# Kernel tuning notes

Hardware: AMD Instinct MI355X
Metric: run time of the kernel (lower is better)

The kernel has to match this reference:

```python
import jax, jax.numpy as jnp
import numpy as np

B, S, E, H = 2, 1024, 1024, 16
Dh = E // H


def setup_inputs() -> dict:
    key = jax.random.key(0)
    ks = jax.random.split(key, 32)
    sc = 1.0 / np.sqrt(E)  # xavier-ish scale
    inp = {}
    names_x = ["x_q_a", "x_q_b", "x_kv_a", "x_kv_b"]
    for i, n in enumerate(names_x):
        inp[n] = jax.random.normal(ks[i], (B, S, E), jnp.float32)
    # causal mask, broadcastable to (B, H, S, S); masked where == 0
    inp["mask"] = jnp.tril(jnp.ones((S, S), jnp.int32))[None, None, :, :]
    inp["layer_theta"] = jnp.float32(0.3)
    inp["thetas_head"] = 0.1 * jax.random.normal(ks[4], (H,), jnp.float32)
    i = 5
    for p in ["q", "k", "v", "o"]:
        inp[p + "_wa"] = sc * jax.random.normal(ks[i], (E, E), jnp.float32); i += 1
        inp[p + "_wb"] = sc * jax.random.normal(ks[i], (E, E), jnp.float32); i += 1
        inp[p + "_ba"] = jnp.zeros((E,), jnp.float32)
        inp[p + "_bb"] = jnp.zeros((E,), jnp.float32)
    return inp


def _qc_dense(xa, xb, wa, wb, ba, bb, j2):
    # F.linear: x @ W.T + b ; j2 is a scalar so (Wb*j2) factors out
    out_a = xa @ wa.T + ba + (xb @ wb.T) * j2
    out_b = xa @ wb.T + bb + xb @ wa.T
    return out_a, out_b


def _shape(x):
    # (B,S,E) -> (B,H,S,Dh)
    return x.reshape(B, S, H, Dh).transpose(0, 2, 1, 3)


def _unshape(x):
    return x.transpose(0, 2, 1, 3).reshape(B, S, E)


def _rope(x):
    # standard rotate-half RoPE on last dim, positions over axis -2
    inv_freq = 1.0 / (10000.0 ** (jnp.arange(0, Dh, 2, dtype=jnp.float32) / Dh))
    ang = jnp.arange(S, dtype=jnp.float32)[:, None] * inv_freq[None, :]  # (S, Dh/2)
    cos = jnp.concatenate([jnp.cos(ang), jnp.cos(ang)], axis=-1)  # (S, Dh)
    sin = jnp.concatenate([jnp.sin(ang), jnp.sin(ang)], axis=-1)
    x1, x2 = x[..., : Dh // 2], x[..., Dh // 2:]
    rot = jnp.concatenate([-x2, x1], axis=-1)
    return x * cos + rot * sin


def reference(x_q_a, x_q_b, x_kv_a, x_kv_b, mask, layer_theta, thetas_head,
              q_wa, q_wb, q_ba, q_bb, k_wa, k_wb, k_ba, k_bb,
              v_wa, v_wb, v_ba, v_bb, o_wa, o_wb, o_ba, o_bb):
    j2 = jnp.sin(2.0 * layer_theta) - 1.0
    qa, qb = _qc_dense(x_q_a, x_q_b, q_wa, q_wb, q_ba, q_bb, j2)
    ka, kb = _qc_dense(x_kv_a, x_kv_b, k_wa, k_wb, k_ba, k_bb, j2)
    va, vb = _qc_dense(x_kv_a, x_kv_b, v_wa, v_wb, v_ba, v_bb, j2)
    qa, qb = _rope(_shape(qa)), _rope(_shape(qb))
    ka, kb = _rope(_shape(ka)), _rope(_shape(kb))
    va, vb = _shape(va), _shape(vb)
    j2h = (jnp.sin(2.0 * thetas_head) - 1.0).reshape(1, H, 1, 1)
    # dual QC score matrices (B,H,S,S)
    s_a = jnp.einsum("bhqd,bhkd->bhqk", qa, ka) + jnp.einsum("bhqd,bhkd->bhqk", qb, kb) * j2h
    s_b = jnp.einsum("bhqd,bhkd->bhqk", qa, kb) + jnp.einsum("bhqd,bhkd->bhqk", qb, ka)
    mag = jnp.sqrt(s_a * s_a + s_b * s_b + 1e-8) / np.sqrt(Dh)
    mag = jnp.where(mask == 0, -1e9, mag)
    attn = jax.nn.softmax(mag, axis=-1)
    out_a = _unshape(jnp.einsum("bhqk,bhkd->bhqd", attn, va))
    out_b = _unshape(jnp.einsum("bhqk,bhkd->bhqd", attn, vb))
    return _qc_dense(out_a, out_b, o_wa, o_wb, o_ba, o_bb, j2)
```

## Files before the change

kernel.cpp:

```cpp
#include <hip/hip_runtime.h>
#include <math.h>
#include <stdint.h>

#define BATCH 2
#define SEQ   1024
#define EMB   1024
#define NH    16
#define DH    64
#define BSE   (BATCH*SEQ*EMB)
#define MROWS (BATCH*SEQ)

typedef unsigned short u16;
typedef __attribute__((ext_vector_type(8))) short short8;
typedef __attribute__((ext_vector_type(4))) float f32x4;

__device__ __forceinline__ float bf2f(u16 u) {
    return __uint_as_float(((unsigned int)u) << 16);
}
__device__ __forceinline__ u16 f2bf(float f) {
    unsigned int x = __float_as_uint(f);
    x += 0x7FFFu + ((x >> 16) & 1u);
    return (u16)(x >> 16);
}

__device__ __forceinline__ void async_copy16(const void* g, void* l) {
    __builtin_amdgcn_global_load_lds(
        (const __attribute__((address_space(1))) unsigned int*)g,
        (__attribute__((address_space(3))) unsigned int*)l,
        16, 0, 0);
}

struct PackArgs {
    const float* src[16];
    u16*         dst[16];
    int          n[16];
    int          scaled[16];
};

__global__ __launch_bounds__(256) void pack_kernel(PackArgs pa, const float* __restrict__ theta)
{
    const int e = blockIdx.y;
    const int i = (blockIdx.x * 256 + threadIdx.x) * 4;
    if (i >= pa.n[e]) return;
    float sc = 1.0f;
    if (pa.scaled[e]) sc = sinf(2.0f * theta[0]) - 1.0f;
    float4 v = *(const float4*)(pa.src[e] + i);
    u16* d = pa.dst[e] + i;
    ushort4 o;
    o.x = f2bf(v.x * sc); o.y = f2bf(v.y * sc);
    o.z = f2bf(v.z * sc); o.w = f2bf(v.w * sc);
    *(ushort4*)d = o;
}

struct GemmArgs {
    const u16*   A1;
    const u16*   A2;
    const u16*   Blo[4];
    const u16*   Bhi[4];
    const float* bias[4];
    void*        dst[4];
    int          mode[4];
};

__global__ __launch_bounds__(256) void mfma_gemm(GemmArgs ga)
{
    __shared__ u16 sA[128][32];
    __shared__ u16 sB[128][32];

    const int t    = threadIdx.x;
    const int lane = t & 63;
    const int w    = t >> 6;
    const int wx   = w & 1;
    const int wy   = w >> 1;
    const int n0   = blockIdx.x * 128;
    const int m0   = blockIdx.y * 128;
    const int seg  = n0 >> 10;
    const int nloc = n0 & 1023;

    const int srow = t >> 2;
    const int sb   = (t & 3) * 16;

    f32x4 acc[4][4] = {};

    const char* A1 = (const char*)ga.A1;
    const char* A2 = (const char*)ga.A2;
    const char* Bl = (const char*)ga.Blo[seg];
    const char* Bh = (const char*)ga.Bhi[seg];

    const int frow = lane & 15;
    const int quad = lane >> 4;

    for (int kt = 0; kt < 64; ++kt) {
        const char* As = (kt & 32) ? A2 : A1;
        const char* Bs = (kt & 32) ? Bh : Bl;
        const size_t kbyte = (size_t)(kt & 31) * 64;

        __syncthreads();
        #pragma unroll
        for (int r = 0; r < 2; ++r) {
            const int row = r*64 + srow;
            const int ldsoff = (r*64 + w*16) * 64;
            async_copy16(As + (size_t)(m0 + row)*2048 + kbyte + sb,
                         (char*)&sA[0][0] + ldsoff);
            async_copy16(Bs + (size_t)(nloc + row)*2048 + kbyte + sb,
                         (char*)&sB[0][0] + ldsoff);
        }
        __syncthreads();

        short8 af[4], bfr[4];
        #pragma unroll
        for (int i = 0; i < 4; ++i)
            af[i] = *(const short8*)&sA[wy*64 + i*16 + frow][quad*8];
        #pragma unroll
        for (int j = 0; j < 4; ++j)
            bfr[j] = *(const short8*)&sB[wx*64 + j*16 + frow][quad*8];

        #pragma unroll
        for (int i = 0; i < 4; ++i)
            #pragma unroll
            for (int j = 0; j < 4; ++j)
                acc[i][j] = __builtin_amdgcn_mfma_f32_16x16x32_bf16(
                                af[i], bfr[j], acc[i][j], 0, 0, 0);
    }

    const float* bias = ga.bias[seg];
    const int mode = ga.mode[seg];
    #pragma unroll
    for (int j = 0; j < 4; ++j) {
        const int c = nloc + wx*64 + j*16 + frow;
        const float bv = bias[c];
        #pragma unroll
        for (int i = 0; i < 4; ++i) {
            #pragma unroll
            for (int reg = 0; reg < 4; ++reg) {
                const int m = m0 + wy*64 + i*16 + quad*4 + reg;
                const float val = acc[i][j][reg] + bv;
                if (mode == 1) {
                    ((float*)ga.dst[seg])[(size_t)m*1024 + c] = val;
                } else if (mode == 2) {
                    ((u16*)ga.dst[seg])[((size_t)(m >> 10) << 20) + (size_t)c*1024 + (m & 1023)] = f2bf(val);
                } else {
                    ((u16*)ga.dst[seg])[(size_t)m*1024 + c] = f2bf(val);
                }
            }
        }
    }
}

__global__ __launch_bounds__(256) void rope_kernel(
    u16* qa, u16* qb, u16* ka, u16* kb)
{
    u16* p;
    switch (blockIdx.y) {
        case 0:  p = qa; break;
        case 1:  p = qb; break;
        case 2:  p = ka; break;
        default: p = kb; break;
    }
    const int i   = blockIdx.x * 256 + threadIdx.x;
    const int d   = i & 31;
    const int hh  = (i >> 5) & (NH - 1);
    const int row = i >> 9;
    const int s   = row & (SEQ - 1);
    const size_t base = (size_t)row * EMB + hh * DH;

    float x1 = bf2f(p[base + d]);
    float x2 = bf2f(p[base + d + 32]);
    const float invf = expf(-(float)d * (9.210340371976184f / 32.0f));
    const float ang  = (float)s * invf;
    float sn, cs;
    sincosf(ang, &sn, &cs);
    p[base + d]      = f2bf(x1 * cs - x2 * sn);
    p[base + d + 32] = f2bf(x2 * cs + x1 * sn);
}

__global__ __launch_bounds__(256) void attn_mfma(
    const u16* __restrict__ qa, const u16* __restrict__ qb,
    const u16* __restrict__ ka, const u16* __restrict__ kb,
    const u16* __restrict__ vat, const u16* __restrict__ vbt,
    const float* __restrict__ thetas,
    u16* __restrict__ oa, u16* __restrict__ ob)
{
    __shared__ u16 sKa[64][64];
    __shared__ u16 sKb[64][64];
    __shared__ u16 sVa[64][64];
    __shared__ u16 sVb[64][64];
    __shared__ u16 sP[4][16][72];

    const int t    = threadIdx.x;
    const int lane = t & 63;
    const int w    = t >> 6;
    const int L15  = lane & 15;
    const int quad = lane >> 4;

    const int bid  = blockIdx.x;
    const int aa   = (bid >> 5) & 7;
    const int qt   = (bid >> 8) ? aa : (15 - aa);
    const int bh   = bid & 31;
    const int h    = bh & 15;
    const int b    = bh >> 4;

    const float j2h = sinf(2.0f * thetas[h]) - 1.0f;

    const int   qrow  = qt*64 + w*16 + L15;
    const size_t qbase = (size_t)(b*SEQ + qrow) * EMB + h*DH;
    short8 fqa[2], fqb[2], fjqb[2];
    fqa[0] = *(const short8*)(qa + qbase + quad*8);
    fqa[1] = *(const short8*)(qa + qbase + 32 + quad*8);
    fqb[0] = *(const short8*)(qb + qbase + quad*8);
    fqb[1] = *(const short8*)(qb + qbase + 32 + quad*8);
    #pragma unroll
    for (int s2 = 0; s2 < 2; ++s2) {
        short8 src = fqb[s2], dst;
        #pragma unroll
        for (int j = 0; j < 8; ++j)
            dst[j] = (short)f2bf(bf2f((u16)src[j]) * j2h);
        fjqb[s2] = dst;
    }

    f32x4 acc_a[4] = {};
    f32x4 acc_b[4] = {};
    float m_run[4] = {-1e30f, -1e30f, -1e30f, -1e30f};
    float l_run[4] = {0.f, 0.f, 0.f, 0.f};

    const int subrow = lane >> 3;
    const int g      = (lane & 7) ^ subrow;
    const int swz    = L15 & 7;

    for (int kt = 0; kt <= qt; ++kt) {
        __syncthreads();
        #pragma unroll
        for (int i = 0; i < 2; ++i) {
            const int row = w*16 + i*8 + subrow;
            const int ldsoff = (w*16 + i*8) * 128;
            const size_t ktok = (size_t)(b*SEQ + kt*64 + row);
            async_copy16((const char*)ka + ktok*2048 + h*128 + g*16,
                         (char*)&sKa[0][0] + ldsoff);
            async_copy16((const char*)kb + ktok*2048 + h*128 + g*16,
                         (char*)&sKb[0][0] + ldsoff);
            const size_t vrow = (size_t)b*1048576 + (size_t)(h*64 + row)*1024 + kt*64;
            async_copy16((const char*)vat + vrow*2 + g*16,
                         (char*)&sVa[0][0] + ldsoff);
            async_copy16((const char*)vbt + vrow*2 + g*16,
                         (char*)&sVb[0][0] + ldsoff);
        }
        __syncthreads();

        f32x4 sa[4] = {}, sb[4] = {};
        #pragma unroll
        for (int n = 0; n < 4; ++n) {
            const u16* rKa = &sKa[n*16 + L15][0];
            const u16* rKb = &sKb[n*16 + L15][0];
            short8 ka0 = *(const short8*)(rKa + (( quad      ^ swz) << 3));
            short8 ka1 = *(const short8*)(rKa + (((4 + quad) ^ swz) << 3));
            short8 kb0 = *(const short8*)(rKb + (( quad      ^ swz) << 3));
            short8 kb1 = *(const short8*)(rKb + (((4 + quad) ^ swz) << 3));
            sa[n] = __builtin_amdgcn_mfma_f32_16x16x32_bf16(fqa[0],  ka0, sa[n], 0, 0, 0);
            sa[n] = __builtin_amdgcn_mfma_f32_16x16x32_bf16(fqa[1],  ka1, sa[n], 0, 0, 0);
            sa[n] = __builtin_amdgcn_mfma_f32_16x16x32_bf16(fjqb[0], kb0, sa[n], 0, 0, 0);
            sa[n] = __builtin_amdgcn_mfma_f32_16x16x32_bf16(fjqb[1], kb1, sa[n], 0, 0, 0);
            sb[n] = __builtin_amdgcn_mfma_f32_16x16x32_bf16(fqa[0],  kb0, sb[n], 0, 0, 0);
            sb[n] = __builtin_amdgcn_mfma_f32_16x16x32_bf16(fqa[1],  kb1, sb[n], 0, 0, 0);
            sb[n] = __builtin_amdgcn_mfma_f32_16x16x32_bf16(fqb[0],  ka0, sb[n], 0, 0, 0);
            sb[n] = __builtin_amdgcn_mfma_f32_16x16x32_bf16(fqb[1],  ka1, sb[n], 0, 0, 0);
        }

        float mag[4][4];
        #pragma unroll
        for (int n = 0; n < 4; ++n)
            #pragma unroll
            for (int r = 0; r < 4; ++r) {
                const float A = sa[n][r], B = sb[n][r];
                mag[n][r] = sqrtf(A*A + B*B + 1e-8f) * 0.125f;
            }
        if (kt == qt) {
            #pragma unroll
            for (int n = 0; n < 4; ++n)
                #pragma unroll
                for (int r = 0; r < 4; ++r)
                    if (n*16 + L15 > w*16 + quad*4 + r) mag[n][r] = -1e9f;
        }

        float rmax[4], psum[4], alpha[4];
        #pragma unroll
        for (int r = 0; r < 4; ++r) {
            float mx = fmaxf(fmaxf(mag[0][r], mag[1][r]), fmaxf(mag[2][r], mag[3][r]));
            #pragma unroll
            for (int off = 8; off >= 1; off >>= 1)
                mx = fmaxf(mx, __shfl_xor(mx, off, 64));
            rmax[r] = mx;
        }
        float p[4][4];
        #pragma unroll
        for (int r = 0; r < 4; ++r) {
            const float m_new = fmaxf(m_run[r], rmax[r]);
            alpha[r] = expf(m_run[r] - m_new);
            m_run[r] = m_new;
            float ps = 0.f;
            #pragma unroll
            for (int n = 0; n < 4; ++n) {
                p[n][r] = expf(mag[n][r] - m_new);
                ps += p[n][r];
            }
            #pragma unroll
            for (int off = 8; off >= 1; off >>= 1)
                ps += __shfl_xor(ps, off, 64);
            psum[r] = ps;
            l_run[r] = l_run[r] * alpha[r] + psum[r];
        }
        #pragma unroll
        for (int n = 0; n < 4; ++n)
            #pragma unroll
            for (int r = 0; r < 4; ++r) {
                acc_a[n][r] *= alpha[r];
                acc_b[n][r] *= alpha[r];
            }

        #pragma unroll
        for (int n = 0; n < 4; ++n)
            #pragma unroll
            for (int r = 0; r < 4; ++r)
                sP[w][quad*4 + r][n*16 + L15] = f2bf(p[n][r]);

        short8 pf0 = *(const short8*)&sP[w][L15][quad*8];
        short8 pf1 = *(const short8*)&sP[w][L15][32 + quad*8];

        #pragma unroll
        for (int n = 0; n < 4; ++n) {
            const u16* rVa = &sVa[n*16 + L15][0];
            const u16* rVb = &sVb[n*16 + L15][0];
            short8 va0 = *(const short8*)(rVa + (( quad      ^ swz) << 3));
            short8 va1 = *(const short8*)(rVa + (((4 + quad) ^ swz) << 3));
            short8 vb0 = *(const short8*)(rVb + (( quad      ^ swz) << 3));
            short8 vb1 = *(const short8*)(rVb + (((4 + quad) ^ swz) << 3));
            acc_a[n] = __builtin_amdgcn_mfma_f32_16x16x32_bf16(pf0, va0, acc_a[n], 0, 0, 0);
            acc_a[n] = __builtin_amdgcn_mfma_f32_16x16x32_bf16(pf1, va1, acc_a[n], 0, 0, 0);
            acc_b[n] = __builtin_amdgcn_mfma_f32_16x16x32_bf16(pf0, vb0, acc_b[n], 0, 0, 0);
            acc_b[n] = __builtin_amdgcn_mfma_f32_16x16x32_bf16(pf1, vb1, acc_b[n], 0, 0, 0);
        }
    }

    float inv[4];
    #pragma unroll
    for (int r = 0; r < 4; ++r) inv[r] = 1.0f / l_run[r];
    #pragma unroll
    for (int reg = 0; reg < 4; ++reg) {
        const size_t tok = (size_t)(b*SEQ + qt*64 + w*16 + quad*4 + reg);
        #pragma unroll
        for (int n = 0; n < 4; ++n) {
            const size_t idx = tok*EMB + h*DH + n*16 + L15;
            oa[idx] = f2bf(acc_a[n][reg] * inv[reg]);
            ob[idx] = f2bf(acc_b[n][reg] * inv[reg]);
        }
    }
}

extern "C" void kernel_launch(void* const* d_in, const int* in_sizes, int n_in,
                              void* d_out, int out_size, void* d_ws, size_t ws_size,
                              hipStream_t stream)
{
    const float* x_q_a  = (const float*)d_in[0];
    const float* x_q_b  = (const float*)d_in[1];
    const float* x_kv_a = (const float*)d_in[2];
    const float* x_kv_b = (const float*)d_in[3];
    const float* theta    = (const float*)d_in[5];
    const float* thetas_h = (const float*)d_in[6];
    const float* q_wa = (const float*)d_in[7];
    const float* q_wb = (const float*)d_in[8];
    const float* q_ba = (const float*)d_in[9];
    const float* q_bb = (const float*)d_in[10];
    const float* k_wa = (const float*)d_in[11];
    const float* k_wb = (const float*)d_in[12];
    const float* k_ba = (const float*)d_in[13];
    const float* k_bb = (const float*)d_in[14];
    const float* v_wa = (const float*)d_in[15];
    const float* v_wb = (const float*)d_in[16];
    const float* v_ba = (const float*)d_in[17];
    const float* v_bb = (const float*)d_in[18];
    const float* o_wa = (const float*)d_in[19];
    const float* o_wb = (const float*)d_in[20];
    const float* o_ba = (const float*)d_in[21];
    const float* o_bb = (const float*)d_in[22];

    u16* W = (u16*)d_ws;
    const size_t XN = (size_t)BSE;
    const size_t WN = (size_t)EMB*EMB;
    u16* xq_a16  = W;
    u16* xq_b16  = W + XN;
    u16* xkv_a16 = W + 2*XN;
    u16* xkv_b16 = W + 3*XN;
    u16* wbase   = W + 4*XN;
    u16* q_wa16  = wbase;
    u16* q_wb16  = wbase + WN;
    u16* k_wa16  = wbase + 2*WN;
    u16* k_wb16  = wbase + 3*WN;
    u16* v_wa16  = wbase + 4*WN;
    u16* v_wb16  = wbase + 5*WN;
    u16* o_wa16  = wbase + 6*WN;
    u16* o_wb16  = wbase + 7*WN;
    u16* q_wbs16 = wbase + 8*WN;
    u16* k_wbs16 = wbase + 9*WN;
    u16* v_wbs16 = wbase + 10*WN;
    u16* o_wbs16 = wbase + 11*WN;
    u16* qkv     = wbase + 12*WN;
    u16* qa16 = qkv;
    u16* qb16 = qkv + XN;
    u16* ka16 = qkv + 2*XN;
    u16* kb16 = qkv + 3*XN;
    u16* vat16 = qkv + 4*XN;
    u16* vbt16 = qkv + 5*XN;
    u16* ao16 = xq_a16;
    u16* bo16 = xq_b16;

    float* out_a = (float*)d_out;
    float* out_b = out_a + (size_t)BSE;

    PackArgs pa;
    const float* psrc[16] = { x_q_a, x_q_b, x_kv_a, x_kv_b,
                              q_wa, q_wb, k_wa, k_wb, v_wa, v_wb, o_wa, o_wb,
                              q_wb, k_wb, v_wb, o_wb };
    u16* pdst[16] = { xq_a16, xq_b16, xkv_a16, xkv_b16,
                      q_wa16, q_wb16, k_wa16, k_wb16, v_wa16, v_wb16, o_wa16, o_wb16,
                      q_wbs16, k_wbs16, v_wbs16, o_wbs16 };
    for (int e = 0; e < 16; ++e) {
        pa.src[e] = psrc[e];
        pa.dst[e] = pdst[e];
        pa.n[e]   = (e < 4) ? (int)XN : (int)WN;
        pa.scaled[e] = (e >= 12) ? 1 : 0;
    }
    pack_kernel<<<dim3(XN/(256*4), 16), 256, 0, stream>>>(pa, theta);

    GemmArgs g1;
    g1.A1 = xq_a16; g1.A2 = xq_b16;
    g1.Blo[0] = q_wa16;  g1.Bhi[0] = q_wbs16; g1.bias[0] = q_ba; g1.dst[0] = qa16; g1.mode[0] = 0;
    g1.Blo[1] = q_wb16;  g1.Bhi[1] = q_wa16;  g1.bias[1] = q_bb; g1.dst[1] = qb16; g1.mode[1] = 0;
    g1.Blo[2] = q_wa16;  g1.Bhi[2] = q_wa16;  g1.bias[2] = q_ba; g1.dst[2] = qa16; g1.mode[2] = 0;
    g1.Blo[3] = q_wa16;  g1.Bhi[3] = q_wa16;  g1.bias[3] = q_ba; g1.dst[3] = qa16; g1.mode[3] = 0;
    mfma_gemm<<<dim3(16, MROWS/128), 256, 0, stream>>>(g1);

    GemmArgs g2;
    g2.A1 = xkv_a16; g2.A2 = xkv_b16;
    g2.Blo[0] = k_wa16; g2.Bhi[0] = k_wbs16; g2.bias[0] = k_ba; g2.dst[0] = ka16;  g2.mode[0] = 0;
    g2.Blo[1] = k_wb16; g2.Bhi[1] = k_wa16;  g2.bias[1] = k_bb; g2.dst[1] = kb16;  g2.mode[1] = 0;
    g2.Blo[2] = v_wa16; g2.Bhi[2] = v_wbs16; g2.bias[2] = v_ba; g2.dst[2] = vat16; g2.mode[2] = 2;
    g2.Blo[3] = v_wb16; g2.Bhi[3] = v_wa16;  g2.bias[3] = v_bb; g2.dst[3] = vbt16; g2.mode[3] = 2;
    mfma_gemm<<<dim3(32, MROWS/128), 256, 0, stream>>>(g2);

    rope_kernel<<<dim3((BATCH*SEQ*NH*32)/256, 4), 256, 0, stream>>>(qa16, qb16, ka16, kb16);

    attn_mfma<<<BATCH*NH*(SEQ/64), 256, 0, stream>>>(qa16, qb16, ka16, kb16,
                                                     vat16, vbt16, thetas_h, ao16, bo16);

    GemmArgs g3;
    g3.A1 = ao16; g3.A2 = bo16;
    g3.Blo[0] = o_wa16; g3.Bhi[0] = o_wbs16; g3.bias[0] = o_ba; g3.dst[0] = out_a; g3.mode[0] = 1;
    g3.Blo[1] = o_wb16; g3.Bhi[1] = o_wa16;  g3.bias[1] = o_bb; g3.dst[1] = out_b; g3.mode[1] = 1;
    g3.Blo[2] = o_wa16; g3.Bhi[2] = o_wa16;  g3.bias[2] = o_ba; g3.dst[2] = out_a; g3.mode[2] = 1;
    g3.Blo[3] = o_wa16; g3.Bhi[3] = o_wa16;  g3.bias[3] = o_ba; g3.dst[3] = out_a; g3.mode[3] = 1;
    mfma_gemm<<<dim3(16, MROWS/128), 256, 0, stream>>>(g3);
}
```

Before: 355.4 us.

## Fuse RoPE into projection GEMM epilogue and merge Q/KV projection launches

Applies rotary embedding directly on the fp32 accumulators in the GEMM epilogue for the Q and K outputs, removing the separate rope kernel and its extra read/write pass over four bf16 tensors. GemmArgs now carries per-segment A operands, so the Q and KV projections run as one launch with 48 column segments. This cuts launch overhead and tail effects, at the cost of sincos work in the epilogue and a larger argument struct.

```diff
diff --git a/kernel.cpp b/kernel.cpp
--- a/kernel.cpp
+++ b/kernel.cpp
@@ -53,13 +53,13 @@
 }
 
 struct GemmArgs {
-    const u16*   A1;
-    const u16*   A2;
-    const u16*   Blo[4];
-    const u16*   Bhi[4];
-    const float* bias[4];
-    void*        dst[4];
-    int          mode[4];
+    const u16*   A1s[8];
+    const u16*   A2s[8];
+    const u16*   Blo[8];
+    const u16*   Bhi[8];
+    const float* bias[8];
+    void*        dst[8];
+    int          mode[8];
 };
 
 __global__ __launch_bounds__(256) void mfma_gemm(GemmArgs ga)
@@ -82,8 +82,8 @@
 
     f32x4 acc[4][4] = {};
 
-    const char* A1 = (const char*)ga.A1;
-    const char* A2 = (const char*)ga.A2;
+    const char* A1 = (const char*)ga.A1s[seg];
+    const char* A2 = (const char*)ga.A2s[seg];
     const char* Bl = (const char*)ga.Blo[seg];
     const char* Bh = (const char*)ga.Bhi[seg];
 
@@ -125,16 +125,48 @@
 
     const float* bias = ga.bias[seg];
     const int mode = ga.mode[seg];
+
     #pragma unroll
     for (int j = 0; j < 4; ++j) {
         const int c = nloc + wx*64 + j*16 + frow;
         const float bv = bias[c];
         #pragma unroll
+        for (int i = 0; i < 4; ++i)
+            #pragma unroll
+            for (int reg = 0; reg < 4; ++reg)
+                acc[i][j][reg] += bv;
+    }
+
+    if (mode == 3) {
+        #pragma unroll
+        for (int jj = 0; jj < 2; ++jj) {
+            const float invf = expf(-(float)(jj*16 + frow) * 0.28782313662425576f);
+            #pragma unroll
+            for (int i = 0; i < 4; ++i) {
+                #pragma unroll
+                for (int reg = 0; reg < 4; ++reg) {
+                    const int m = m0 + wy*64 + i*16 + quad*4 + reg;
+                    const float ang = (float)(m & (SEQ-1)) * invf;
+                    float sn, cs;
+                    sincosf(ang, &sn, &cs);
+                    const float x1 = acc[i][jj][reg];
+                    const float x2 = acc[i][jj+2][reg];
+                    acc[i][jj][reg]   = x1*cs - x2*sn;
+                    acc[i][jj+2][reg] = x2*cs + x1*sn;
+                }
+            }
+        }
+    }
+
+    #pragma unroll
+    for (int j = 0; j < 4; ++j) {
+        const int c = nloc + wx*64 + j*16 + frow;
+        #pragma unroll
         for (int i = 0; i < 4; ++i) {
             #pragma unroll
             for (int reg = 0; reg < 4; ++reg) {
                 const int m = m0 + wy*64 + i*16 + quad*4 + reg;
-                const float val = acc[i][j][reg] + bv;
+                const float val = acc[i][j][reg];
                 if (mode == 1) {
                     ((float*)ga.dst[seg])[(size_t)m*1024 + c] = val;
                 } else if (mode == 2) {
@@ -145,33 +177,6 @@
             }
         }
     }
-}
-
-__global__ __launch_bounds__(256) void rope_kernel(
-    u16* qa, u16* qb, u16* ka, u16* kb)
-{
-    u16* p;
-    switch (blockIdx.y) {
-        case 0:  p = qa; break;
-        case 1:  p = qb; break;
-        case 2:  p = ka; break;
-        default: p = kb; break;
-    }
-    const int i   = blockIdx.x * 256 + threadIdx.x;
-    const int d   = i & 31;
-    const int hh  = (i >> 5) & (NH - 1);
-    const int row = i >> 9;
-    const int s   = row & (SEQ - 1);
-    const size_t base = (size_t)row * EMB + hh * DH;
-
-    float x1 = bf2f(p[base + d]);
-    float x2 = bf2f(p[base + d + 32]);
-    const float invf = expf(-(float)d * (9.210340371976184f / 32.0f));
-    const float ang  = (float)s * invf;
-    float sn, cs;
-    sincosf(ang, &sn, &cs);
-    p[base + d]      = f2bf(x1 * cs - x2 * sn);
-    p[base + d + 32] = f2bf(x2 * cs + x1 * sn);
 }
 
 __global__ __launch_bounds__(256) void attn_mfma(
@@ -430,32 +435,35 @@
     }
     pack_kernel<<<dim3(XN/(256*4), 16), 256, 0, stream>>>(pa, theta);
 
-    GemmArgs g1;
-    g1.A1 = xq_a16; g1.A2 = xq_b16;
-    g1.Blo[0] = q_wa16;  g1.Bhi[0] = q_wbs16; g1.bias[0] = q_ba; g1.dst[0] = qa16; g1.mode[0] = 0;
-    g1.Blo[1] = q_wb16;  g1.Bhi[1] = q_wa16;  g1.bias[1] = q_bb; g1.dst[1] = qb16; g1.mode[1] = 0;
-    g1.Blo[2] = q_wa16;  g1.Bhi[2] = q_wa16;  g1.bias[2] = q_ba; g1.dst[2] = qa16; g1.mode[2] = 0;
-    g1.Blo[3] = q_wa16;  g1.Bhi[3] = q_wa16;  g1.bias[3] = q_ba; g1.dst[3] = qa16; g1.mode[3] = 0;
-    mfma_gemm<<<dim3(16, MROWS/128), 256, 0, stream>>>(g1);
-
-    GemmArgs g2;
-    g2.A1 = xkv_a16; g2.A2 = xkv_b16;
-    g2.Blo[0] = k_wa16; g2.Bhi[0] = k_wbs16; g2.bias[0] = k_ba; g2.dst[0] = ka16;  g2.mode[0] = 0;
-    g2.Blo[1] = k_wb16; g2.Bhi[1] = k_wa16;  g2.bias[1] = k_bb; g2.dst[1] = kb16;  g2.mode[1] = 0;
-    g2.Blo[2] = v_wa16; g2.Bhi[2] = v_wbs16; g2.bias[2] = v_ba; g2.dst[2] = vat16; g2.mode[2] = 2;
-    g2.Blo[3] = v_wb16; g2.Bhi[3] = v_wa16;  g2.bias[3] = v_bb; g2.dst[3] = vbt16; g2.mode[3] = 2;
-    mfma_gemm<<<dim3(32, MROWS/128), 256, 0, stream>>>(g2);
-
-    rope_kernel<<<dim3((BATCH*SEQ*NH*32)/256, 4), 256, 0, stream>>>(qa16, qb16, ka16, kb16);
+    GemmArgs g12;
+    const u16* a1s[6] = { xq_a16, xq_a16, xkv_a16, xkv_a16, xkv_a16, xkv_a16 };
+    const u16* a2s[6] = { xq_b16, xq_b16, xkv_b16, xkv_b16, xkv_b16, xkv_b16 };
+    const u16* blo[6] = { q_wa16, q_wb16, k_wa16, k_wb16, v_wa16, v_wb16 };
+    const u16* bhi[6] = { q_wbs16, q_wa16, k_wbs16, k_wa16, v_wbs16, v_wa16 };
+    const float* bia[6] = { q_ba, q_bb, k_ba, k_bb, v_ba, v_bb };
+    void* dsts[6] = { qa16, qb16, ka16, kb16, vat16, vbt16 };
+    const int modes[6] = { 3, 3, 3, 3, 2, 2 };
+    for (int s = 0; s < 6; ++s) {
+        g12.A1s[s] = a1s[s]; g12.A2s[s] = a2s[s];
+        g12.Blo[s] = blo[s]; g12.Bhi[s] = bhi[s];
+        g12.bias[s] = bia[s]; g12.dst[s] = dsts[s]; g12.mode[s] = modes[s];
+    }
+    for (int s = 6; s < 8; ++s) {
+        g12.A1s[s] = a1s[0]; g12.A2s[s] = a2s[0];
+        g12.Blo[s] = blo[0]; g12.Bhi[s] = bhi[0];
+        g12.bias[s] = bia[0]; g12.dst[s] = dsts[0]; g12.mode[s] = 0;
+    }
+    mfma_gemm<<<dim3(48, MROWS/128), 256, 0, stream>>>(g12);
 
     attn_mfma<<<BATCH*NH*(SEQ/64), 256, 0, stream>>>(qa16, qb16, ka16, kb16,
                                                      vat16, vbt16, thetas_h, ao16, bo16);
 
     GemmArgs g3;
-    g3.A1 = ao16; g3.A2 = bo16;
-    g3.Blo[0] = o_wa16; g3.Bhi[0] = o_wbs16; g3.bias[0] = o_ba; g3.dst[0] = out_a; g3.mode[0] = 1;
-    g3.Blo[1] = o_wb16; g3.Bhi[1] = o_wa16;  g3.bias[1] = o_bb; g3.dst[1] = out_b; g3.mode[1] = 1;
-    g3.Blo[2] = o_wa16; g3.Bhi[2] = o_wa16;  g3.bias[2] = o_ba; g3.dst[2] = out_a; g3.mode[2] = 1;
-    g3.Blo[3] = o_wa16; g3.Bhi[3] = o_wa16;  g3.bias[3] = o_ba; g3.dst[3] = out_a; g3.mode[3] = 1;
+    for (int s = 0; s < 8; ++s) {
+        g3.A1s[s] = ao16; g3.A2s[s] = bo16;
+        g3.Blo[s] = o_wa16; g3.Bhi[s] = o_wbs16;
+        g3.bias[s] = o_ba; g3.dst[s] = out_a; g3.mode[s] = 1;
+    }
+    g3.Blo[1] = o_wb16; g3.Bhi[1] = o_wa16; g3.bias[1] = o_bb; g3.dst[1] = out_b;
     mfma_gemm<<<dim3(16, MROWS/128), 256, 0, stream>>>(g3);
 }
```

Measured after the change: 344.7 us. -3.0%, faster.
